# Performance work log

Hardware: AMD Instinct MI355X
Metric: run time of the kernel (lower is better)

Reference implementation:

```python
import jax, jax.numpy as jnp
import numpy as np

N_EMBD = 1024
HEAD_SIZE = 64


def setup_inputs() -> dict:
    key = jax.random.key(0)
    kx, kq, kk, kv = jax.random.split(key, 4)
    B, T = 8, 2048
    x = jax.random.normal(kx, (B, T, N_EMBD), dtype=jnp.float32)
    s = 1.0 / np.sqrt(N_EMBD)
    Wq = jax.random.normal(kq, (N_EMBD, HEAD_SIZE), dtype=jnp.float32) * s
    Wk = jax.random.normal(kk, (N_EMBD, HEAD_SIZE), dtype=jnp.float32) * s
    Wv = jax.random.normal(kv, (N_EMBD, HEAD_SIZE), dtype=jnp.float32) * s
    return {"x": x, "Wq": Wq, "Wk": Wk, "Wv": Wv}


def reference(x, Wq, Wk, Wv):
    # x: [B, T, C]; W*: [C, H]
    q = jnp.einsum('btc,ch->bth', x, Wq)
    k = jnp.einsum('btc,ch->bth', x, Wk)
    v = jnp.einsum('btc,ch->bth', x, Wv)
    H = q.shape[-1]
    score = jnp.einsum('bth,bsh->bts', q, k) / jnp.sqrt(jnp.asarray(H, q.dtype))
    T = score.shape[-1]
    causal = jnp.tril(jnp.ones((T, T), dtype=bool))  # [T, T]
    score = jnp.where(causal, score, -jnp.inf)
    attn = jax.nn.softmax(score, axis=-1)
    return jnp.einsum('bts,bsh->bth', attn, v)
```

## Files before the change

### kernel.cpp

```cpp
#include <hip/hip_runtime.h>

typedef __bf16 bf16;
typedef __attribute__((ext_vector_type(8))) __bf16 bf16x8;
typedef __attribute__((ext_vector_type(4))) __bf16 bf16x4;
typedef __attribute__((ext_vector_type(4))) float floatx4;

#define MFMA16(a, b, c) __builtin_amdgcn_mfma_f32_16x16x32_bf16((a), (b), (c), 0, 0, 0)

__global__ void prep_w(const float* __restrict__ Wq, const float* __restrict__ Wk,
                       const float* __restrict__ Wv, bf16* __restrict__ wTf) {
    int tid = blockIdx.x * 256 + threadIdx.x;
    int j = tid & 7;
    int l = (tid >> 3) & 15;
    int q = (tid >> 7) & 3;
    int kc = (tid >> 9) & 31;
    int mt = tid >> 14;
    int mat = mt >> 2;
    int h = ((mt & 3) << 4) + l;
    int c = kc * 32 + q * 8 + j;
    const float* W = (mat == 0) ? Wq : (mat == 1) ? Wk : Wv;
    wTf[tid] = (bf16)W[c * 64 + h];
}

__global__ __launch_bounds__(256, 2) void proj_qkv(const float* __restrict__ x,
                                                   const bf16* __restrict__ wTf,
                                                   bf16* __restrict__ q,
                                                   bf16* __restrict__ k,
                                                   bf16* __restrict__ vT) {
    __shared__ __align__(16) char xsb[32 * 2048];

    const int tid = threadIdx.x;
    const int lane = tid & 63;
    const int w = tid >> 6;
    const int l15 = lane & 15;
    const int quad = lane >> 4;
    const int T0 = blockIdx.x * 32;

    {
        const int r = tid >> 4;
        const int cm = tid & 15;
        #pragma unroll
        for (int half = 0; half < 2; half++) {
            const int row = r + half * 16;
            const float* g = x + (size_t)(T0 + row) * 1024 + cm * 8;
            floatx4 f[16];
            #pragma unroll
            for (int c = 0; c < 8; c++) {
                f[2 * c]     = *(const floatx4*)(g + c * 128);
                f[2 * c + 1] = *(const floatx4*)(g + c * 128 + 4);
            }
            char* ldb = xsb + row * 2048;
            const int sxs = (row & 7) << 4;
            #pragma unroll
            for (int c = 0; c < 8; c++) {
                bf16x8 pk;
                pk[0] = (bf16)f[2*c][0]; pk[1] = (bf16)f[2*c][1];
                pk[2] = (bf16)f[2*c][2]; pk[3] = (bf16)f[2*c][3];
                pk[4] = (bf16)f[2*c+1][0]; pk[5] = (bf16)f[2*c+1][1];
                pk[6] = (bf16)f[2*c+1][2]; pk[7] = (bf16)f[2*c+1][3];
                *(bf16x8*)(ldb + ((cm * 16 + c * 256) ^ sxs)) = pk;
            }
        }
    }
    __syncthreads();

    floatx4 acc[6] = {};
    const bf16* aw0 = wTf + (size_t)(w * 3 + 0) * 16384 + lane * 8;
    const bf16* aw1 = wTf + (size_t)(w * 3 + 1) * 16384 + lane * 8;
    const bf16* aw2 = wTf + (size_t)(w * 3 + 2) * 16384 + lane * 8;
    const char* xr = xsb + l15 * 2048;
    const int sx = (l15 & 7) << 4;
    const int q16 = quad * 16;

    bf16x8 a0c = *(const bf16x8*)(aw0);
    bf16x8 a1c = *(const bf16x8*)(aw1);
    bf16x8 a2c = *(const bf16x8*)(aw2);
    bf16x8 a0n = *(const bf16x8*)(aw0 + 512);
    bf16x8 a1n = *(const bf16x8*)(aw1 + 512);
    bf16x8 a2n = *(const bf16x8*)(aw2 + 512);

    #pragma unroll 4
    for (int kc = 0; kc < 32; kc++) {
        bf16x8 p0 = *(const bf16x8*)(aw0 + (kc + 2) * 512);
        bf16x8 p1 = *(const bf16x8*)(aw1 + (kc + 2) * 512);
        bf16x8 p2 = *(const bf16x8*)(aw2 + (kc + 2) * 512);
        const int o = (kc * 64 + q16) ^ sx;
        bf16x8 b0 = *(const bf16x8*)(xr + o);
        bf16x8 b1 = *(const bf16x8*)(xr + 32768 + o);
        acc[0] = MFMA16(a0c, b0, acc[0]);
        acc[1] = MFMA16(a0c, b1, acc[1]);
        acc[2] = MFMA16(a1c, b0, acc[2]);
        acc[3] = MFMA16(a1c, b1, acc[3]);
        acc[4] = MFMA16(a2c, b0, acc[4]);
        acc[5] = MFMA16(a2c, b1, acc[5]);
        a0c = a0n; a1c = a1n; a2c = a2n;
        a0n = p0;  a1n = p1;  a2n = p2;
    }

    #pragma unroll
    for (int i = 0; i < 3; i++) {
        int mtile = w * 3 + i;
        int mat = mtile >> 2;
        int hbase = ((mtile & 3) << 4) + (quad << 2);
        float sc = (mat == 0) ? 0.18033688011112042f : 1.0f;
        #pragma unroll
        for (int tt = 0; tt < 2; tt++) {
            const int t = T0 + tt * 16 + l15;
            floatx4 av = acc[i * 2 + tt];
            bf16x4 pk;
            pk[0] = (bf16)(av[0] * sc);
            pk[1] = (bf16)(av[1] * sc);
            pk[2] = (bf16)(av[2] * sc);
            pk[3] = (bf16)(av[3] * sc);
            if (mat == 0) {
                *(bf16x4*)(q + (size_t)t * 64 + hbase) = pk;
            } else if (mat == 1) {
                *(bf16x4*)(k + (size_t)t * 64 + hbase) = pk;
            } else {
                int bidx = t >> 11, tmod = t & 2047;
                #pragma unroll
                for (int r = 0; r < 4; r++)
                    vT[(size_t)(bidx * 64 + hbase + r) * 2048 + tmod] = pk[r];
            }
        }
    }
}

#define KP2 72
#define OH 68

__global__ __launch_bounds__(512, 4) void flash(const bf16* __restrict__ q,
                                                const bf16* __restrict__ k,
                                                const bf16* __restrict__ vT,
                                                float* __restrict__ out) {
    __shared__ char smem[8 * 16 * OH * 4];
    __shared__ float Ms[8][16], Ls[8][16];
    bf16* psall = (bf16*)smem;
    float* Os = (float*)smem;

    const int b = blockIdx.x & 7;
    const int p = blockIdx.x >> 3;
    const int t0A = p * 16;
    const int t0B = (127 - p) * 16;
    const int nttA = (p >> 2) + 1;
    const int nttB = ((127 - p) >> 2) + 1;
    const int L = nttA + nttB;

    const int tid = threadIdx.x;
    const int w = tid >> 6;
    const int lane = tid & 63;
    const int l15 = lane & 15;
    const int quad = lane >> 4;

    const int s0 = (L * w) >> 3;
    const int s1 = (L * (w + 1)) >> 3;

    const bf16* kbase = k + (size_t)(b * 2048 + l15) * 64 + quad * 8;
    const bf16* vbase = vT + (size_t)(b * 64 + l15) * 2048 + quad * 8;
    bf16* psw = psall + w * 16 * KP2;

    const bf16* qpA = q + (size_t)(b * 2048 + t0A + l15) * 64 + quad * 8;
    const bf16* qpB = q + (size_t)(b * 2048 + t0B + l15) * 64 + quad * 8;

    floatx4 oA[4] = {}, oB[4] = {};
    float miA = -1e30f, liA = 0.f, miB = -1e30f, liB = 0.f;

#define KV_STEP(jtv, isdiag, t0v, qf0v, qf1v, mi_, li_, o_)                          \
    {                                                                                 \
        const bf16* kp = kbase + (size_t)(jtv) * 4096;                                \
        floatx4 stt[4];                                                               \
        __builtin_amdgcn_s_setprio(1);                                                \
        _Pragma("unroll") for (int mt = 0; mt < 4; mt++) {                            \
            floatx4 z = {};                                                           \
            bf16x8 ka0 = *(const bf16x8*)(kp + mt * 1024);                            \
            bf16x8 ka1 = *(const bf16x8*)(kp + mt * 1024 + 32);                       \
            z = MFMA16(ka0, qf0v, z);                                                 \
            z = MFMA16(ka1, qf1v, z);                                                 \
            stt[mt] = z;                                                              \
        }                                                                             \
        __builtin_amdgcn_s_setprio(0);                                                \
        if (isdiag) {                                                                 \
            _Pragma("unroll") for (int mt = 0; mt < 4; mt++)                          \
                _Pragma("unroll") for (int r = 0; r < 4; r++) {                       \
                    int kv = (jtv) * 64 + mt * 16 + quad * 4 + r;                     \
                    if (kv > (t0v) + l15) stt[mt][r] = -1e30f;                        \
                }                                                                     \
        }                                                                             \
        float mx = fmaxf(fmaxf(fmaxf(stt[0][0], stt[0][1]), fmaxf(stt[0][2], stt[0][3])),  \
                         fmaxf(fmaxf(stt[1][0], stt[1][1]), fmaxf(stt[1][2], stt[1][3]))); \
        mx = fmaxf(mx, fmaxf(fmaxf(fmaxf(stt[2][0], stt[2][1]), fmaxf(stt[2][2], stt[2][3])),  \
                             fmaxf(fmaxf(stt[3][0], stt[3][1]), fmaxf(stt[3][2], stt[3][3])))); \
        mx = fmaxf(mx, __shfl_xor(mx, 16, 64));                                       \
        mx = fmaxf(mx, __shfl_xor(mx, 32, 64));                                       \
        const bool nodefer = !__all(mx - mi_ <= 8.0f);                                \
        const float mnew = nodefer ? fmaxf(mi_, mx) : mi_;                            \
        float rs = 0.f;                                                               \
        _Pragma("unroll") for (int mt = 0; mt < 4; mt++)                              \
            _Pragma("unroll") for (int r = 0; r < 4; r++) {                           \
                float pv = __builtin_amdgcn_exp2f(stt[mt][r] - mnew);                 \
                stt[mt][r] = pv;                                                      \
                rs += pv;                                                             \
            }                                                                         \
        rs += __shfl_xor(rs, 16, 64);                                                 \
        rs += __shfl_xor(rs, 32, 64);                                                 \
        if (nodefer) {                                                                \
            const float aa = __builtin_amdgcn_exp2f(mi_ - mnew);                      \
            mi_ = mnew;                                                               \
            li_ *= aa;                                                                \
            _Pragma("unroll") for (int mt = 0; mt < 4; mt++)                          \
                _Pragma("unroll") for (int r = 0; r < 4; r++) o_[mt][r] *= aa;        \
        }                                                                             \
        li_ += rs;                                                                    \
        _Pragma("unroll") for (int mt = 0; mt < 4; mt++) {                            \
            bf16x4 pk;                                                                \
            pk[0] = (bf16)stt[mt][0]; pk[1] = (bf16)stt[mt][1];                       \
            pk[2] = (bf16)stt[mt][2]; pk[3] = (bf16)stt[mt][3];                       \
            *(bf16x4*)(psw + l15 * KP2 + mt * 16 + quad * 4) = pk;                    \
        }                                                                             \
        const bf16* vp = vbase + (jtv) * 64;                                          \
        __builtin_amdgcn_s_setprio(1);                                                \
        _Pragma("unroll") for (int kc = 0; kc < 2; kc++) {                            \
            bf16x8 pb = *(const bf16x8*)(psw + l15 * KP2 + kc * 32 + quad * 8);       \
            _Pragma("unroll") for (int mt = 0; mt < 4; mt++) {                        \
                bf16x8 va = *(const bf16x8*)(vp + mt * 32768 + kc * 32);              \
                o_[mt] = MFMA16(va, pb, o_[mt]);                                      \
            }                                                                         \
        }                                                                             \
        __builtin_amdgcn_s_setprio(0);                                                \
    }

    {
        const int eA = (s1 < nttA) ? s1 : nttA;
        if (s0 < eA) {
            bf16x8 qf0 = *(const bf16x8*)qpA;
            bf16x8 qf1 = *(const bf16x8*)(qpA + 32);
            for (int s = s0; s < eA; s++) {
                KV_STEP(s, (s == nttA - 1), t0A, qf0, qf1, miA, liA, oA);
            }
        }
    }
    {
        const int sB = (s0 > nttA) ? s0 : nttA;
        if (sB < s1) {
            bf16x8 qf0 = *(const bf16x8*)qpB;
            bf16x8 qf1 = *(const bf16x8*)(qpB + 32);
            for (int s = sB; s < s1; s++) {
                KV_STEP(s - nttA, (s == L - 1), t0B, qf0, qf1, miB, liB, oB);
            }
        }
    }

    #pragma unroll
    for (int tile = 0; tile < 2; tile++) {
        __syncthreads();
        float mi = tile ? miB : miA;
        float li = tile ? liB : liA;
        if (lane < 16) { Ms[w][lane] = mi; Ls[w][lane] = li; }
        #pragma unroll
        for (int mt = 0; mt < 4; mt++) {
            floatx4 ov = tile ? oB[mt] : oA[mt];
            *(floatx4*)(Os + (w * 16 + l15) * OH + mt * 16 + quad * 4) = ov;
        }
        __syncthreads();
        {
            int qq = tid >> 5;
            int h2 = (tid & 31) * 2;
            float Mg = -1e30f;
            #pragma unroll
            for (int u = 0; u < 8; u++) Mg = fmaxf(Mg, Ms[u][qq]);
            float Lg = 0.f, v0 = 0.f, v1 = 0.f;
            #pragma unroll
            for (int u = 0; u < 8; u++) {
                float sw = __builtin_amdgcn_exp2f(Ms[u][qq] - Mg);
                Lg += sw * Ls[u][qq];
                const float* Or = Os + (u * 16 + qq) * OH + h2;
                v0 += sw * Or[0];
                v1 += sw * Or[1];
            }
            float inv = 1.0f / Lg;
            int t0v = tile ? t0B : t0A;
            float* op = out + (size_t)(b * 2048 + t0v + qq) * 64 + h2;
            op[0] = v0 * inv;
            op[1] = v1 * inv;
        }
    }
#undef KV_STEP
}

extern "C" void kernel_launch(void* const* d_in, const int* in_sizes, int n_in,
                              void* d_out, int out_size, void* d_ws, size_t ws_size,
                              hipStream_t stream) {
    const float* x  = (const float*)d_in[0];
    const float* Wq = (const float*)d_in[1];
    const float* Wk = (const float*)d_in[2];
    const float* Wv = (const float*)d_in[3];
    float* out = (float*)d_out;

    char* ws = (char*)d_ws;
    bf16* wTf = (bf16*)ws;
    bf16* q   = (bf16*)(ws + 397312);
    bf16* k   = (bf16*)(ws + 397312 + 2097152);
    bf16* vT  = (bf16*)(ws + 397312 + 2 * 2097152);

    hipLaunchKernelGGL(prep_w,   dim3(768), dim3(256), 0, stream, Wq, Wk, Wv, wTf);
    hipLaunchKernelGGL(proj_qkv, dim3(512), dim3(256), 0, stream, x, wTf, q, k, vT);
    hipLaunchKernelGGL(flash,    dim3(512), dim3(512), 0, stream, q, k, vT, out);
}
```

Before: 140.0 us.

## Stream x tiles into LDS chunk-by-chunk during projection MFMA loop

The QKV projection kernel used to load and convert the whole 32x1024 fp32 x tile into LDS before starting any MFMA work. It now loads x in 64-column chunks with two chunks of register prefetch, and converts and stores the next chunk while the current one is multiplied. A barrier per chunk keeps LDS consistent. This is meant to hide global-load latency behind compute, at the cost of sixteen barriers per block. Separately, the attention row-max reduction is regrouped into three-input fmaxf groups so the compiler can emit max3 instructions.

```diff
diff --git a/kernel.cpp b/kernel.cpp
--- a/kernel.cpp
+++ b/kernel.cpp
@@ -36,32 +36,29 @@
     const int quad = lane >> 4;
     const int T0 = blockIdx.x * 32;
 
-    {
-        const int r = tid >> 4;
-        const int cm = tid & 15;
-        #pragma unroll
-        for (int half = 0; half < 2; half++) {
-            const int row = r + half * 16;
-            const float* g = x + (size_t)(T0 + row) * 1024 + cm * 8;
-            floatx4 f[16];
-            #pragma unroll
-            for (int c = 0; c < 8; c++) {
-                f[2 * c]     = *(const floatx4*)(g + c * 128);
-                f[2 * c + 1] = *(const floatx4*)(g + c * 128 + 4);
-            }
-            char* ldb = xsb + row * 2048;
-            const int sxs = (row & 7) << 4;
-            #pragma unroll
-            for (int c = 0; c < 8; c++) {
-                bf16x8 pk;
-                pk[0] = (bf16)f[2*c][0]; pk[1] = (bf16)f[2*c][1];
-                pk[2] = (bf16)f[2*c][2]; pk[3] = (bf16)f[2*c][3];
-                pk[4] = (bf16)f[2*c+1][0]; pk[5] = (bf16)f[2*c+1][1];
-                pk[6] = (bf16)f[2*c+1][2]; pk[7] = (bf16)f[2*c+1][3];
-                *(bf16x8*)(ldb + ((cm * 16 + c * 256) ^ sxs)) = pk;
-            }
-        }
-    }
+    const int srow = tid >> 3;
+    const int scg = tid & 7;
+    const float* sg = x + (size_t)(T0 + srow) * 1024 + scg * 8;
+    char* sld = xsb + srow * 2048;
+    const int sws = (srow & 7) << 4;
+
+#define STC(c, f0, f1)                                                          \
+    {                                                                            \
+        bf16x8 pk;                                                               \
+        pk[0] = (bf16)(f0)[0]; pk[1] = (bf16)(f0)[1];                            \
+        pk[2] = (bf16)(f0)[2]; pk[3] = (bf16)(f0)[3];                            \
+        pk[4] = (bf16)(f1)[0]; pk[5] = (bf16)(f1)[1];                            \
+        pk[6] = (bf16)(f1)[2]; pk[7] = (bf16)(f1)[3];                            \
+        *(bf16x8*)(sld + (((c) * 128 + scg * 16) ^ sws)) = pk;                   \
+    }
+
+    floatx4 A0 = *(const floatx4*)(sg);
+    floatx4 A1 = *(const floatx4*)(sg + 4);
+    floatx4 B0 = *(const floatx4*)(sg + 64);
+    floatx4 B1 = *(const floatx4*)(sg + 68);
+    floatx4 C0 = *(const floatx4*)(sg + 128);
+    floatx4 C1 = *(const floatx4*)(sg + 132);
+    STC(0, A0, A1);
     __syncthreads();
 
     floatx4 acc[6] = {};
@@ -79,23 +76,36 @@
     bf16x8 a1n = *(const bf16x8*)(aw1 + 512);
     bf16x8 a2n = *(const bf16x8*)(aw2 + 512);
 
-    #pragma unroll 4
-    for (int kc = 0; kc < 32; kc++) {
-        bf16x8 p0 = *(const bf16x8*)(aw0 + (kc + 2) * 512);
-        bf16x8 p1 = *(const bf16x8*)(aw1 + (kc + 2) * 512);
-        bf16x8 p2 = *(const bf16x8*)(aw2 + (kc + 2) * 512);
-        const int o = (kc * 64 + q16) ^ sx;
-        bf16x8 b0 = *(const bf16x8*)(xr + o);
-        bf16x8 b1 = *(const bf16x8*)(xr + 32768 + o);
-        acc[0] = MFMA16(a0c, b0, acc[0]);
-        acc[1] = MFMA16(a0c, b1, acc[1]);
-        acc[2] = MFMA16(a1c, b0, acc[2]);
-        acc[3] = MFMA16(a1c, b1, acc[3]);
-        acc[4] = MFMA16(a2c, b0, acc[4]);
-        acc[5] = MFMA16(a2c, b1, acc[5]);
-        a0c = a0n; a1c = a1n; a2c = a2n;
-        a0n = p0;  a1n = p1;  a2n = p2;
-    }
+    #pragma unroll
+    for (int c = 0; c < 16; c++) {
+        floatx4 N0 = {}, N1 = {};
+        if (c < 13) {
+            N0 = *(const floatx4*)(sg + (c + 3) * 64);
+            N1 = *(const floatx4*)(sg + (c + 3) * 64 + 4);
+        }
+        #pragma unroll
+        for (int u = 0; u < 2; u++) {
+            const int kc = 2 * c + u;
+            bf16x8 p0 = *(const bf16x8*)(aw0 + (kc + 2) * 512);
+            bf16x8 p1 = *(const bf16x8*)(aw1 + (kc + 2) * 512);
+            bf16x8 p2 = *(const bf16x8*)(aw2 + (kc + 2) * 512);
+            const int o = (kc * 64 + q16) ^ sx;
+            bf16x8 b0 = *(const bf16x8*)(xr + o);
+            bf16x8 b1 = *(const bf16x8*)(xr + 32768 + o);
+            acc[0] = MFMA16(a0c, b0, acc[0]);
+            acc[1] = MFMA16(a0c, b1, acc[1]);
+            acc[2] = MFMA16(a1c, b0, acc[2]);
+            acc[3] = MFMA16(a1c, b1, acc[3]);
+            acc[4] = MFMA16(a2c, b0, acc[4]);
+            acc[5] = MFMA16(a2c, b1, acc[5]);
+            a0c = a0n; a1c = a1n; a2c = a2n;
+            a0n = p0;  a1n = p1;  a2n = p2;
+        }
+        if (c < 15) STC(c + 1, B0, B1);
+        __syncthreads();
+        B0 = C0; B1 = C1; C0 = N0; C1 = N1;
+    }
+#undef STC
 
     #pragma unroll
     for (int i = 0; i < 3; i++) {
@@ -186,10 +196,13 @@
                     if (kv > (t0v) + l15) stt[mt][r] = -1e30f;                        \
                 }                                                                     \
         }                                                                             \
-        float mx = fmaxf(fmaxf(fmaxf(stt[0][0], stt[0][1]), fmaxf(stt[0][2], stt[0][3])),  \
-                         fmaxf(fmaxf(stt[1][0], stt[1][1]), fmaxf(stt[1][2], stt[1][3]))); \
-        mx = fmaxf(mx, fmaxf(fmaxf(fmaxf(stt[2][0], stt[2][1]), fmaxf(stt[2][2], stt[2][3])),  \
-                             fmaxf(fmaxf(stt[3][0], stt[3][1]), fmaxf(stt[3][2], stt[3][3])))); \
+        float m0_ = fmaxf(fmaxf(stt[0][0], stt[0][1]), stt[0][2]);                    \
+        float m1_ = fmaxf(fmaxf(stt[0][3], stt[1][0]), stt[1][1]);                    \
+        float m2_ = fmaxf(fmaxf(stt[1][2], stt[1][3]), stt[2][0]);                    \
+        float m3_ = fmaxf(fmaxf(stt[2][1], stt[2][2]), stt[2][3]);                    \
+        float m4_ = fmaxf(fmaxf(stt[3][0], stt[3][1]), stt[3][2]);                    \
+        float mx = fmaxf(fmaxf(fmaxf(m0_, m1_), m2_),                                 \
+                         fmaxf(fmaxf(m3_, m4_), stt[3][3]));                          \
         mx = fmaxf(mx, __shfl_xor(mx, 16, 64));                                       \
         mx = fmaxf(mx, __shfl_xor(mx, 32, 64));                                       \
         const bool nodefer = !__all(mx - mi_ <= 8.0f);                                \
```

Result: slower. 144.1 us (+2.9%).
